# Kernel tuning notes

Hardware: AMD Instinct MI355X
Metric: run time of the kernel (lower is better)

The kernel has to match this reference:

```python
import jax, jax.numpy as jnp
import numpy as np

N, E, D = 100000, 640000, 128

def setup_inputs() -> dict:
    key = jax.random.key(0)
    ks = jax.random.split(key, 12)
    s = 1.0 / np.sqrt(D)
    sg = 1.0 / np.sqrt(2 * D)
    return {
        "nodes": jax.random.normal(ks[0], (N, D), jnp.float32),
        "globals_": jax.random.normal(ks[1], (1, D), jnp.float32),
        "senders": jax.random.randint(ks[2], (E,), 0, N, jnp.int32),
        "receivers": jax.random.randint(ks[3], (E,), 0, N, jnp.int32),
        "W1_w": jax.random.normal(ks[4], (D, D), jnp.float32) * s,
        "W1_b": jnp.zeros((D,), jnp.float32),
        "W2_w": jax.random.normal(ks[5], (D, D), jnp.float32) * s,
        "W2_b": jnp.zeros((D,), jnp.float32),
        "W3_w": jax.random.normal(ks[6], (D, D), jnp.float32) * s,
        "W3_b": jnp.zeros((D,), jnp.float32),
        "Wg_w": jax.random.normal(ks[7], (2 * D, D), jnp.float32) * sg,
        "Wg_b": jnp.zeros((D,), jnp.float32),
    }


def reference(nodes, globals_, senders, receivers,
              W1_w, W1_b, W2_w, W2_b, W3_w, W3_b, Wg_w, Wg_b):
    n = nodes.shape[0]
    # W1 skip-branch projection
    h = nodes @ W1_w + W1_b                              # [N, D]
    # GraphConvolution: W2 projection + symmetric-normalized sum aggregation
    conv = nodes @ W2_w + W2_b                           # [N, D]
    ones = jnp.ones(senders.shape, conv.dtype)
    send_deg = jax.ops.segment_sum(ones, senders, num_segments=n)
    recv_deg = jax.ops.segment_sum(ones, receivers, num_segments=n)
    conv = conv * jax.lax.rsqrt(jnp.maximum(send_deg, 1.0))[:, None]
    agg = jax.ops.segment_sum(conv[senders], receivers, num_segments=n)  # gather + scatter
    agg = agg * jax.lax.rsqrt(jnp.maximum(recv_deg, 1.0))[:, None]
    h = h + agg
    # global -> node broadcast (globals is not None)
    h = h + (globals_[0:1] @ W3_w + W3_b)
    h = jax.nn.relu(h)
    h = h + nodes                                        # residual
    # global update: aggregate nodes (sum over single graph) + gated residual
    an = jnp.sum(h, axis=0, keepdims=True)               # [1, D]
    g_new = globals_ + jax.nn.relu(jnp.concatenate([an, globals_], axis=-1) @ Wg_w + Wg_b)
    return h, g_new
```

## Files before the change

kernel.cpp:

```cpp
#include <hip/hip_runtime.h>

#define D 128
#define SCH 1024
#define AGGB 2048

typedef __attribute__((ext_vector_type(8))) short short8;
typedef __attribute__((ext_vector_type(4))) float floatx4;

__device__ inline void bf16split(float x, ushort& hi, ushort& lo) {
  unsigned u = __float_as_uint(x);
  unsigned rh = (u + 0x7FFFu + ((u >> 16) & 1u)) & 0xFFFF0000u;
  hi = (ushort)(rh >> 16);
  float fl = x - __uint_as_float(rh);
  unsigned ul = __float_as_uint(fl);
  lo = (ushort)((ul + 0x7FFFu + ((ul >> 16) & 1u)) >> 16);
}

__global__ void k_front(const int* __restrict__ snd, const int* __restrict__ rcv,
                        int* __restrict__ cs, int* __restrict__ cr, int E, int nbE,
                        const float* __restrict__ g, const float* __restrict__ W3,
                        const float* __restrict__ b3, float* __restrict__ gvec,
                        const float* __restrict__ nodes, ushort* __restrict__ nhl,
                        int n) {
  __shared__ float part[256];
  const int b = blockIdx.x;
  if (b < nbE) {
    const int e = b * 256 + threadIdx.x;
    if (e < E) {
      atomicAdd(cs + snd[e], 1);
      atomicAdd(cr + rcv[e], 1);
    }
    return;
  }
  if (b == nbE) {
    const int j = threadIdx.x & 127, half = threadIdx.x >> 7;
    float acc = 0.f;
    for (int k = half * 64; k < half * 64 + 64; ++k)
      acc = fmaf(g[k], W3[k * D + j], acc);
    part[threadIdx.x] = acc;
    __syncthreads();
    if (threadIdx.x < D) gvec[j] = b3[j] + part[j] + part[j + 128];
    return;
  }
  const int id = (b - nbE - 1) * 256 + threadIdx.x;
  if (id >= n * 16) return;
  const int r = id >> 4, c = (id & 15) * 8;
  const float* gp = nodes + (size_t)r * D + c;
  const float4 v0 = *(const float4*)gp;
  const float4 v1 = *(const float4*)(gp + 4);
  ushort h0, l0, h1, l1, h2, l2, h3, l3;
  ushort* ob = nhl + (size_t)r * 256;
  bf16split(v0.x, h0, l0); bf16split(v0.y, h1, l1);
  bf16split(v0.z, h2, l2); bf16split(v0.w, h3, l3);
  *(ushort4*)(ob + c) = make_ushort4(h0, h1, h2, h3);
  *(ushort4*)(ob + 128 + c) = make_ushort4(l0, l1, l2, l3);
  bf16split(v1.x, h0, l0); bf16split(v1.y, h1, l1);
  bf16split(v1.z, h2, l2); bf16split(v1.w, h3, l3);
  *(ushort4*)(ob + c + 4) = make_ushort4(h0, h1, h2, h3);
  *(ushort4*)(ob + 128 + c + 4) = make_ushort4(l0, l1, l2, l3);
}

__global__ void k_scan(const int* __restrict__ cnt, int* __restrict__ bsum,
                       int* __restrict__ off, int* __restrict__ cursor, int n) {
  __shared__ int sh[256];
  __shared__ int red[4];
  const int t = threadIdx.x, b = blockIdx.x;
  const int base = b * SCH + t * 4;
  int4 v = make_int4(0, 0, 0, 0);
  if (base < n) v = *(const int4*)(cnt + base);
  const int s = v.x + v.y + v.z + v.w;
  sh[t] = s;
  __syncthreads();
  for (int st = 1; st < 256; st <<= 1) {
    const int u = (t >= st) ? sh[t - st] : 0;
    __syncthreads();
    sh[t] += u;
    __syncthreads();
  }
  if (t == 255) atomicExch(bsum + b, sh[255] + 1);
  int pre = 0;
  if (t < b) {
    int x = atomicAdd(bsum + t, 0);
    while (x == 0) {
      __builtin_amdgcn_s_sleep(1);
      x = atomicAdd(bsum + t, 0);
    }
    pre = x - 1;
  }
#pragma unroll
  for (int o = 32; o > 0; o >>= 1) pre += __shfl_down(pre, o, 64);
  if ((t & 63) == 0) red[t >> 6] = pre;
  __syncthreads();
  const int gbase = red[0] + red[1] + red[2] + red[3];
  const int ex = sh[t] - s + gbase;
  if (base < n) {
    const int4 o4 = make_int4(ex, ex + v.x, ex + v.x + v.y, ex + v.x + v.y + v.z);
    *(int4*)(off + base) = o4;
    *(int4*)(cursor + base) = o4;
  }
}

__global__ void k_fill(const int* __restrict__ snd, const int* __restrict__ rcv,
                       int* __restrict__ cursor, int* __restrict__ srt, int E) {
  const int e = blockIdx.x * blockDim.x + threadIdx.x;
  if (e < E) {
    const int p = atomicAdd(cursor + rcv[e], 1);
    srt[p] = snd[e];
  }
}

__global__ __launch_bounds__(256) void k_agg(
    const float* __restrict__ nodes, const int* __restrict__ off,
    int* __restrict__ cnt_recv, const int* __restrict__ cnt_send,
    const int* __restrict__ srt, ushort* __restrict__ yh,
    ushort* __restrict__ yl, int n, const float* __restrict__ W1,
    const float* __restrict__ W2, ushort* __restrict__ wt) {
  if ((int)blockIdx.x >= AGGB) {
    const int id = ((int)blockIdx.x - AGGB) * 256 + threadIdx.x;
    const int mat = id >> 14, idx = id & 16383;
    const int k = idx >> 7, nn = idx & 127;
    const float x = (mat ? W2 : W1)[k * D + nn];
    ushort hi, lo;
    bf16split(x, hi, lo);
    wt[(size_t)mat * 32768 + (size_t)nn * 128 + k] = hi;
    wt[(size_t)mat * 32768 + 16384 + (size_t)nn * 128 + k] = lo;
    return;
  }
  float* cf = (float*)cnt_recv;
  const int hw = threadIdx.x >> 5, ln = threadIdx.x & 31;
  const int ghw = blockIdx.x * 8 + hw;
  const int nhw = AGGB * 8;
  const int c0 = ln * 4;

  for (int r0 = ghw; r0 < n; r0 += 2 * nhw) {
    const int r1 = r0 + nhw;
    const bool has1 = r1 < n;
    const int dg0 = cnt_recv[r0];
    const int o0 = off[r0];
    const int dg1 = has1 ? cnt_recv[r1] : 0;
    const int o1 = has1 ? off[r1] : o0;
    const int safe0 = (dg0 > 0) ? o0 : 0;
    const int safe1 = (dg1 > 0) ? o1 : 0;

    int idx0[8], idx1[8];
#pragma unroll
    for (int j = 0; j < 8; ++j) {
      idx0[j] = srt[safe0 + (j < dg0 ? j : 0)];
      idx1[j] = srt[safe1 + (j < dg1 ? j : 0)];
    }
    float4 g0[8], g1[8];
#pragma unroll
    for (int j = 0; j < 8; ++j)
      g0[j] = *(const float4*)(nodes + (size_t)idx0[j] * D + c0);
#pragma unroll
    for (int j = 0; j < 8; ++j)
      g1[j] = *(const float4*)(nodes + (size_t)idx1[j] * D + c0);
    float rs0[8], rs1[8];
#pragma unroll
    for (int j = 0; j < 8; ++j) {
      rs0[j] = (j < dg0) ? rsqrtf(fmaxf((float)cnt_send[idx0[j]], 1.f)) : 0.f;
      rs1[j] = (j < dg1) ? rsqrtf(fmaxf((float)cnt_send[idx1[j]], 1.f)) : 0.f;
    }

    float sx0 = 0.f, sy0 = 0.f, sz0 = 0.f, sw0 = 0.f, cs0 = 0.f;
    float sx1 = 0.f, sy1 = 0.f, sz1 = 0.f, sw1 = 0.f, cs1 = 0.f;
#pragma unroll
    for (int j = 0; j < 8; ++j) {
      sx0 = fmaf(rs0[j], g0[j].x, sx0);
      sy0 = fmaf(rs0[j], g0[j].y, sy0);
      sz0 = fmaf(rs0[j], g0[j].z, sz0);
      sw0 = fmaf(rs0[j], g0[j].w, sw0);
      cs0 += rs0[j];
      sx1 = fmaf(rs1[j], g1[j].x, sx1);
      sy1 = fmaf(rs1[j], g1[j].y, sy1);
      sz1 = fmaf(rs1[j], g1[j].z, sz1);
      sw1 = fmaf(rs1[j], g1[j].w, sw1);
      cs1 += rs1[j];
    }
    for (int i = 8; i < dg0; ++i) {
      const int s = srt[o0 + i];
      const float r = rsqrtf(fmaxf((float)cnt_send[s], 1.f));
      const float4 c = *(const float4*)(nodes + (size_t)s * D + c0);
      sx0 = fmaf(r, c.x, sx0); sy0 = fmaf(r, c.y, sy0);
      sz0 = fmaf(r, c.z, sz0); sw0 = fmaf(r, c.w, sw0);
      cs0 += r;
    }
    for (int i = 8; i < dg1; ++i) {
      const int s = srt[o1 + i];
      const float r = rsqrtf(fmaxf((float)cnt_send[s], 1.f));
      const float4 c = *(const float4*)(nodes + (size_t)s * D + c0);
      sx1 = fmaf(r, c.x, sx1); sy1 = fmaf(r, c.y, sy1);
      sz1 = fmaf(r, c.z, sz1); sw1 = fmaf(r, c.w, sw1);
      cs1 += r;
    }

    {
      const float rr = rsqrtf(fmaxf((float)dg0, 1.f));
      ushort h0, l0, h1, l1, h2, l2, h3, l3;
      bf16split(sx0 * rr, h0, l0);
      bf16split(sy0 * rr, h1, l1);
      bf16split(sz0 * rr, h2, l2);
      bf16split(sw0 * rr, h3, l3);
      *(ushort4*)(yh + (size_t)r0 * D + c0) = make_ushort4(h0, h1, h2, h3);
      *(ushort4*)(yl + (size_t)r0 * D + c0) = make_ushort4(l0, l1, l2, l3);
      if (ln == 0) cf[r0] = rr * cs0;
    }
    if (has1) {
      const float rr = rsqrtf(fmaxf((float)dg1, 1.f));
      ushort h0, l0, h1, l1, h2, l2, h3, l3;
      bf16split(sx1 * rr, h0, l0);
      bf16split(sy1 * rr, h1, l1);
      bf16split(sz1 * rr, h2, l2);
      bf16split(sw1 * rr, h3, l3);
      *(ushort4*)(yh + (size_t)r1 * D + c0) = make_ushort4(h0, h1, h2, h3);
      *(ushort4*)(yl + (size_t)r1 * D + c0) = make_ushort4(l0, l1, l2, l3);
      if (ln == 0) cf[r1] = rr * cs1;
    }
  }
}

__global__ __launch_bounds__(256, 3) void k_gemm(
    const float* __restrict__ A, const ushort* nhl, const ushort* __restrict__ yh,
    const ushort* __restrict__ yl, const ushort* __restrict__ wt,
    const float* __restrict__ b1, const float* __restrict__ b2,
    const float* __restrict__ gvec, const float* __restrict__ cf,
    float* outH, float* __restrict__ an, int n) {
  const int t = threadIdx.x;
  const int row0 = blockIdx.x * 64;
  const int lane = t & 63, w = t >> 6;
  const int m = lane & 15, quad = lane >> 4;

  floatx4 acc[4][2];
#pragma unroll
  for (int i = 0; i < 4; ++i)
#pragma unroll
    for (int j = 0; j < 2; ++j) acc[i][j] = (floatx4)0.f;

  int rr[4];
#pragma unroll
  for (int i = 0; i < 4; ++i) rr[i] = min(row0 + i * 16 + m, n - 1);

  for (int p = 0; p < 4; ++p) {
    const int kofs = p * 32 + quad * 8;
    short8 a1h[4], a1l[4], a2h[4], a2l[4];
#pragma unroll
    for (int i = 0; i < 4; ++i) {
      const ushort* nb = nhl + (size_t)rr[i] * 256 + kofs;
      a1h[i] = *(const short8*)nb;
      a1l[i] = *(const short8*)(nb + 128);
      const size_t yo = (size_t)rr[i] * D + kofs;
      a2h[i] = *(const short8*)(yh + yo);
      a2l[i] = *(const short8*)(yl + yo);
    }
#pragma unroll
    for (int j = 0; j < 2; ++j) {
      const int col = w * 32 + j * 16 + m;
      const ushort* g1 = wt + (size_t)col * 128 + kofs;
      const short8 w1h = *(const short8*)g1;
      const short8 w1l = *(const short8*)(g1 + 16384);
      const short8 w2h = *(const short8*)(g1 + 32768);
      const short8 w2l = *(const short8*)(g1 + 49152);
#pragma unroll
      for (int i = 0; i < 4; ++i) {
        floatx4 c = acc[i][j];
        c = __builtin_amdgcn_mfma_f32_16x16x32_bf16(a1h[i], w1h, c, 0, 0, 0);
        c = __builtin_amdgcn_mfma_f32_16x16x32_bf16(a1h[i], w1l, c, 0, 0, 0);
        c = __builtin_amdgcn_mfma_f32_16x16x32_bf16(a1l[i], w1h, c, 0, 0, 0);
        c = __builtin_amdgcn_mfma_f32_16x16x32_bf16(a2h[i], w2h, c, 0, 0, 0);
        c = __builtin_amdgcn_mfma_f32_16x16x32_bf16(a2h[i], w2l, c, 0, 0, 0);
        c = __builtin_amdgcn_mfma_f32_16x16x32_bf16(a2l[i], w2h, c, 0, 0, 0);
        acc[i][j] = c;
      }
    }
  }

  __syncthreads();

  float bb[2], b2c[2];
#pragma unroll
  for (int j = 0; j < 2; ++j) {
    const int col = w * 32 + j * 16 + m;
    bb[j] = b1[col] + gvec[col];
    b2c[j] = b2[col];
  }
  float asum[2] = {0.f, 0.f};
#pragma unroll
  for (int i = 0; i < 4; ++i)
#pragma unroll
    for (int pp = 0; pp < 4; ++pp) {
      const int rg = row0 + i * 16 + quad * 4 + pp;
      if (rg >= n) continue;
      const float crv = cf[rg];
#pragma unroll
      for (int j = 0; j < 2; ++j) {
        const int col = w * 32 + j * 16 + m;
        float v = acc[i][j][pp] + bb[j] + crv * b2c[j];
        v = fmaxf(v, 0.f) + A[(size_t)rg * D + col];
        outH[(size_t)rg * D + col] = v;
        asum[j] += v;
      }
    }
#pragma unroll
  for (int j = 0; j < 2; ++j) {
    float v = asum[j];
    v += __shfl_xor(v, 16);
    v += __shfl_xor(v, 32);
    if (lane < 16) atomicAdd(an + w * 32 + j * 16 + m, v);
  }
}

__global__ void k_gupdate(const float* __restrict__ an, const float* __restrict__ g,
                          const float* __restrict__ Wg, const float* __restrict__ bg,
                          float* __restrict__ gout) {
  __shared__ float part[256];
  const int j = threadIdx.x & 127, half = threadIdx.x >> 7;
  float acc = 0.f;
  if (half == 0) {
    for (int k = 0; k < D; ++k) acc = fmaf(an[k], Wg[k * D + j], acc);
  } else {
    for (int k = 0; k < D; ++k) acc = fmaf(g[k], Wg[(D + k) * D + j], acc);
  }
  part[threadIdx.x] = acc;
  __syncthreads();
  if (threadIdx.x < D)
    gout[j] = g[j] + fmaxf(bg[j] + part[j] + part[j + 128], 0.f);
}

extern "C" void kernel_launch(void* const* d_in, const int* in_sizes, int n_in,
                              void* d_out, int out_size, void* d_ws, size_t ws_size,
                              hipStream_t stream) {
  const float* nodes = (const float*)d_in[0];
  const float* globals_ = (const float*)d_in[1];
  const int* senders = (const int*)d_in[2];
  const int* receivers = (const int*)d_in[3];
  const float* W1_w = (const float*)d_in[4];
  const float* W1_b = (const float*)d_in[5];
  const float* W2_w = (const float*)d_in[6];
  const float* W2_b = (const float*)d_in[7];
  const float* W3_w = (const float*)d_in[8];
  const float* W3_b = (const float*)d_in[9];
  const float* Wg_w = (const float*)d_in[10];
  const float* Wg_b = (const float*)d_in[11];
  const int N = in_sizes[0] / D;
  const int E = in_sizes[2];
  const int nb = (N + SCH - 1) / SCH;
  const int nbE = (E + 255) / 256;
  const int nsb = (N * 16 + 255) / 256;

  float* h = (float*)d_out;
  float* gout = h + (size_t)N * D;
  ushort* nhl = (ushort*)d_out;

  float* ws = (float*)d_ws;
  ushort* yh = (ushort*)ws;
  ushort* yl = yh + (size_t)N * D;
  int* cnt_send = (int*)(yl + (size_t)N * D);
  int* cnt_recv = cnt_send + N;
  int* bsum = cnt_recv + N;
  float* an = (float*)(bsum + 256);
  int* off = (int*)(an + D);
  int* cursor = off + N;
  int* srt = cursor + N;
  float* gvec = (float*)(srt + E);
  ushort* wt = (ushort*)cursor;

  (void)hipMemsetAsync(cnt_send, 0, (size_t)(2 * N + 256 + D) * sizeof(int), stream);

  hipLaunchKernelGGL(k_front, dim3(nbE + 1 + nsb), dim3(256), 0, stream,
                     senders, receivers, cnt_send, cnt_recv, E, nbE,
                     globals_, W3_w, W3_b, gvec, nodes, nhl, N);
  hipLaunchKernelGGL(k_scan, dim3(nb), dim3(256), 0, stream,
                     cnt_recv, bsum, off, cursor, N);
  hipLaunchKernelGGL(k_fill, dim3(nbE), dim3(256), 0, stream,
                     senders, receivers, cursor, srt, E);
  hipLaunchKernelGGL(k_agg, dim3(AGGB + 128), dim3(256), 0, stream,
                     nodes, off, cnt_recv, cnt_send, srt, yh, yl, N,
                     W1_w, W2_w, wt);
  hipLaunchKernelGGL(k_gemm, dim3((N + 63) / 64), dim3(256), 0, stream,
                     nodes, nhl, yh, yl, wt, W1_b, W2_b, gvec,
                     (const float*)cnt_recv, h, an, N);
  hipLaunchKernelGGL(k_gupdate, dim3(1), dim3(256), 0, stream, an, globals_,
                     Wg_w, Wg_b, gout);
}
```

Measured before the change: 404.2 us.

## Stage GEMM A tiles through double-buffered LDS with register prefetch

The GEMM kernel now loads the A operands (split-bf16 node and y rows) cooperatively into a double-buffered padded shared-memory tile. It prefetches the next K slice into registers while the current one is used by the MFMAs. Previously each of the four waves re-read the same A rows from global memory, so this targets redundant global traffic and load latency. It adds LDS usage (about 40KB per block), a barrier per K step and a raised occupancy hint, which may pressure LDS capacity or registers.

Result: faster. 376.0 us (-7.0%).

```diff
diff --git a/kernel.cpp b/kernel.cpp
--- a/kernel.cpp
+++ b/kernel.cpp
@@ -219,12 +219,13 @@
   }
 }
 
-__global__ __launch_bounds__(256, 3) void k_gemm(
+__global__ __launch_bounds__(256, 4) void k_gemm(
     const float* __restrict__ A, const ushort* nhl, const ushort* __restrict__ yh,
     const ushort* __restrict__ yl, const ushort* __restrict__ wt,
     const float* __restrict__ b1, const float* __restrict__ b2,
     const float* __restrict__ gvec, const float* __restrict__ cf,
     float* outH, float* __restrict__ an, int n) {
+  __shared__ ushort As[2][4][64 * 40];
   const int t = threadIdx.x;
   const int row0 = blockIdx.x * 64;
   const int lane = t & 63, w = t >> 6;
@@ -236,45 +237,66 @@
 #pragma unroll
     for (int j = 0; j < 2; ++j) acc[i][j] = (floatx4)0.f;
 
-  int rr[4];
-#pragma unroll
-  for (int i = 0; i < 4; ++i) rr[i] = min(row0 + i * 16 + m, n - 1);
+  const int srow = t >> 2, ko = (t & 3) * 8;
+  const int grow = min(row0 + srow, n - 1);
+  const ushort* nb = nhl + (size_t)grow * 256 + ko;
+  const ushort* yhb = yh + (size_t)grow * D + ko;
+  const ushort* ylb = yl + (size_t)grow * D + ko;
+  const int sa = srow * 40 + ko;
+
+  uint4 r0, r1, r2, r3;
+#define LOADP(p)                                   \
+  {                                                \
+    r0 = *(const uint4*)(nb + (p) * 32);           \
+    r1 = *(const uint4*)(nb + 128 + (p) * 32);     \
+    r2 = *(const uint4*)(yhb + (p) * 32);          \
+    r3 = *(const uint4*)(ylb + (p) * 32);          \
+  }
+#define STOREB(buf)                                \
+  {                                                \
+    *(uint4*)&As[buf][0][sa] = r0;                 \
+    *(uint4*)&As[buf][1][sa] = r1;                 \
+    *(uint4*)&As[buf][2][sa] = r2;                 \
+    *(uint4*)&As[buf][3][sa] = r3;                 \
+  }
+
+  LOADP(0);
+  STOREB(0);
+  LOADP(1);
+  __syncthreads();
 
   for (int p = 0; p < 4; ++p) {
-    const int kofs = p * 32 + quad * 8;
-    short8 a1h[4], a1l[4], a2h[4], a2l[4];
-#pragma unroll
-    for (int i = 0; i < 4; ++i) {
-      const ushort* nb = nhl + (size_t)rr[i] * 256 + kofs;
-      a1h[i] = *(const short8*)nb;
-      a1l[i] = *(const short8*)(nb + 128);
-      const size_t yo = (size_t)rr[i] * D + kofs;
-      a2h[i] = *(const short8*)(yh + yo);
-      a2l[i] = *(const short8*)(yl + yo);
-    }
+    if (p < 3) STOREB((p + 1) & 1);
+    if (p < 2) LOADP(p + 2);
+    const ushort* Ab = &As[p & 1][0][0];
 #pragma unroll
     for (int j = 0; j < 2; ++j) {
-      const int col = w * 32 + j * 16 + m;
-      const ushort* g1 = wt + (size_t)col * 128 + kofs;
+      const ushort* g1 = wt + (size_t)(w * 32 + j * 16 + m) * 128 + p * 32 + quad * 8;
       const short8 w1h = *(const short8*)g1;
       const short8 w1l = *(const short8*)(g1 + 16384);
       const short8 w2h = *(const short8*)(g1 + 32768);
       const short8 w2l = *(const short8*)(g1 + 49152);
 #pragma unroll
       for (int i = 0; i < 4; ++i) {
+        const int r = (i * 16 + m) * 40 + quad * 8;
+        const short8 a1h = *(const short8*)&Ab[r];
+        const short8 a1l = *(const short8*)&Ab[2560 + r];
+        const short8 a2h = *(const short8*)&Ab[5120 + r];
+        const short8 a2l = *(const short8*)&Ab[7680 + r];
         floatx4 c = acc[i][j];
-        c = __builtin_amdgcn_mfma_f32_16x16x32_bf16(a1h[i], w1h, c, 0, 0, 0);
-        c = __builtin_amdgcn_mfma_f32_16x16x32_bf16(a1h[i], w1l, c, 0, 0, 0);
-        c = __builtin_amdgcn_mfma_f32_16x16x32_bf16(a1l[i], w1h, c, 0, 0, 0);
-        c = __builtin_amdgcn_mfma_f32_16x16x32_bf16(a2h[i], w2h, c, 0, 0, 0);
-        c = __builtin_amdgcn_mfma_f32_16x16x32_bf16(a2h[i], w2l, c, 0, 0, 0);
-        c = __builtin_amdgcn_mfma_f32_16x16x32_bf16(a2l[i], w2h, c, 0, 0, 0);
+        c = __builtin_amdgcn_mfma_f32_16x16x32_bf16(a1h, w1h, c, 0, 0, 0);
+        c = __builtin_amdgcn_mfma_f32_16x16x32_bf16(a1h, w1l, c, 0, 0, 0);
+        c = __builtin_amdgcn_mfma_f32_16x16x32_bf16(a1l, w1h, c, 0, 0, 0);
+        c = __builtin_amdgcn_mfma_f32_16x16x32_bf16(a2h, w2h, c, 0, 0, 0);
+        c = __builtin_amdgcn_mfma_f32_16x16x32_bf16(a2h, w2l, c, 0, 0, 0);
+        c = __builtin_amdgcn_mfma_f32_16x16x32_bf16(a2l, w2h, c, 0, 0, 0);
         acc[i][j] = c;
       }
     }
-  }
-
-  __syncthreads();
+    __syncthreads();
+  }
+#undef LOADP
+#undef STOREB
 
   float bb[2], b2c[2];
 #pragma unroll
```
